# Optimization experiments

Measured on AMD Instinct MI355X. Metric: run time of the kernel, lower is better.

The kernel has to match this reference:

```python
import jax, jax.numpy as jnp
import numpy as np
import math

HID = 128
NH = 8
HD = HID // NH
NL = 3
CLIP = 10.0
EPS = 1e-5

def _ln(x, g, b):
    mu = jnp.mean(x, axis=-1, keepdims=True)
    var = jnp.var(x, axis=-1, keepdims=True)
    return (x - mu) * jax.lax.rsqrt(var + EPS) * g + b

def _layer(h, e_bias1, e_gate2, g1, b1, wh, g2, b2, w1, w2):
    B, N, _ = h.shape
    h_in = h
    hn = _ln(h, g1, b1)
    qkv = hn @ wh                                   # (B,N,3H)
    q, k, v = jnp.split(qkv, 3, axis=-1)
    q = q.reshape(B, N, NH, HD).transpose(0, 2, 1, 3)  # (B,nh,N,hd)
    k = k.reshape(B, N, NH, HD).transpose(0, 2, 1, 3)
    v = v.reshape(B, N, NH, HD).transpose(0, 2, 1, 3)
    att = jnp.einsum('bhid,bhjd->bhij', q, k) * (1.0 / math.sqrt(HD))
    att = jax.nn.softmax(att + e_bias1, axis=-1) * e_gate2
    y = jnp.einsum('bhij,bhjd->bhid', att, v)
    y = y.transpose(0, 2, 1, 3).reshape(B, N, HID)
    z = _ln(y + h_in, g2, b2)
    mlp = jax.nn.relu(z @ w1) @ w2
    return mlp + y

def setup_inputs() -> dict:
    key = jax.random.key(0)
    ks = jax.random.split(key, 9)
    d = {
        'node_features': jax.random.normal(ks[0], (16, 256, 2), jnp.float32),
        'edge_features': jax.random.normal(ks[1], (16, 256, 256, 1), jnp.float32),
        'Wn': jax.random.normal(ks[2], (2, HID), jnp.float32) * 0.5,
        'We_in': jax.random.normal(ks[3], (1, HID), jnp.float32) * 0.1,
        'ln1_g': jnp.ones((NL, HID), jnp.float32),
        'ln1_b': jnp.zeros((NL, HID), jnp.float32),
        'Wh': jax.random.normal(ks[4], (NL, HID, 3 * HID), jnp.float32) * (1.0 / math.sqrt(HID)),
        'We': jax.random.normal(ks[5], (NL, HID, 2 * NH), jnp.float32) * (1.0 / math.sqrt(HID)),
        'ln2_g': jnp.ones((NL, HID), jnp.float32),
        'ln2_b': jnp.zeros((NL, HID), jnp.float32),
        'W1': jax.random.normal(ks[6], (NL, HID, 4 * HID), jnp.float32) * (1.0 / math.sqrt(HID)),
        'W2': jax.random.normal(ks[7], (NL, 4 * HID, HID), jnp.float32) * (1.0 / math.sqrt(4 * HID)),
        'Wdec': jax.random.normal(ks[8], (HID, 1), jnp.float32) * (1.0 / math.sqrt(HID)),
    }
    return d

def reference(node_features, edge_features, Wn, We_in, ln1_g, ln1_b, Wh, We, ln2_g, ln2_b, W1, W2, Wdec):
    h = node_features @ Wn                              # (B,N,H)
    e = edge_features @ We_in                           # (B,N,N,H)
    for i in range(NL):
        ee = e @ We[i]                                  # (B,N,N,2*nh)
        ee = ee.transpose(0, 3, 1, 2)                   # (B,2*nh,N,N)
        e1, e2 = ee[:, :NH], ee[:, NH:]
        h = _layer(h, e1, e2, ln1_g[i], ln1_b[i], Wh[i], ln2_g[i], ln2_b[i], W1[i], W2[i])
    out = h @ Wdec                                      # (B,N,1)
    out = CLIP * jnp.tanh(out / math.sqrt(HID))
    return out
```

## Files before the change

### kernel.cpp

```cpp
#include <hip/hip_runtime.h>
#include <math.h>

#define HID 128
#define NHEAD 8
#define NL 3
#define NS 256
#define ROWS 4096

typedef __attribute__((ext_vector_type(8))) short bf16x8;
typedef __attribute__((ext_vector_type(4))) float f32x4;

__device__ __forceinline__ float us2f(unsigned short s) { return __uint_as_float(((unsigned)s) << 16); }
__device__ __forceinline__ unsigned short f2b(float f) {
    unsigned u = __float_as_uint(f);
    return (unsigned short)((u + 0x7fff + ((u >> 16) & 1)) >> 16);
}

__global__ __launch_bounds__(256) void k_prep(
    const float* __restrict__ Wh, const float* __restrict__ W1, const float* __restrict__ W2,
    const float* __restrict__ We_in, const float* __restrict__ We,
    const float* __restrict__ nf, const float* __restrict__ Wn,
    unsigned short* __restrict__ WhH, unsigned short* __restrict__ WhL,
    unsigned short* __restrict__ W1H, unsigned short* __restrict__ W1L,
    unsigned short* __restrict__ W2H, unsigned short* __restrict__ W2L,
    float* __restrict__ sbuf, float* __restrict__ h)
{
    int b = blockIdx.x, t = threadIdx.x;
    if (b >= 529) {
        int idx = (b - 529) * 256 + t;
        int r = idx >> 7, c = idx & 127;
        h[idx] = nf[2 * r] * Wn[c] + nf[2 * r + 1] * Wn[HID + c];
        return;
    }
    if (b == 528) {
        if (t < NL * 2 * NHEAD) {
            int l = t / (2 * NHEAD), j = t % (2 * NHEAD);
            float acc = 0.f;
            for (int c = 0; c < HID; ++c)
                acc += We_in[c] * We[(long)(l * HID + c) * (2 * NHEAD) + j];
            sbuf[t] = acc;
        }
        return;
    }
    const float* S; unsigned short *OH, *OL; int K, N, kt, nt;
    if (b < 144) {
        int l = b / 48, rem = b % 48; kt = rem & 3; nt = rem >> 2; K = 128; N = 384;
        S = Wh + (long)l * 128 * 384; OH = WhH + (long)l * 384 * 128; OL = WhL + (long)l * 384 * 128;
    } else if (b < 336) {
        int b2 = b - 144; int l = b2 / 64, rem = b2 % 64; kt = rem & 3; nt = rem >> 2; K = 128; N = 512;
        S = W1 + (long)l * 128 * 512; OH = W1H + (long)l * 512 * 128; OL = W1L + (long)l * 512 * 128;
    } else {
        int b2 = b - 336; int l = b2 / 64, rem = b2 % 64; kt = rem & 15; nt = rem >> 4; K = 512; N = 128;
        S = W2 + (long)l * 512 * 128; OH = W2H + (long)l * 128 * 512; OL = W2L + (long)l * 128 * 512;
    }
    __shared__ float sm[32][33];
    int i0 = t >> 5, j = t & 31;
#pragma unroll
    for (int p = 0; p < 4; ++p) {
        int i = i0 + p * 8;
        sm[i][j] = S[(long)(kt * 32 + i) * N + nt * 32 + j];
    }
    __syncthreads();
#pragma unroll
    for (int p = 0; p < 4; ++p) {
        int n = i0 + p * 8;
        float v = sm[j][n];
        unsigned short hh = f2b(v);
        long o = (long)(nt * 32 + n) * K + kt * 32 + j;
        OH[o] = hh; OL[o] = f2b(v - us2f(hh));
    }
}

__global__ __launch_bounds__(256) void k_fgemm(
    const float* __restrict__ x, const float* __restrict__ x2,
    const float* __restrict__ g, const float* __restrict__ b,
    const unsigned short* __restrict__ WH, const unsigned short* __restrict__ WL,
    unsigned short* __restrict__ Ch, unsigned short* __restrict__ Cl,
    int Nc, int mode)
{
    __shared__ unsigned short sAh[64 * 136], sAl[64 * 136];
    __shared__ unsigned short sWh[64 * 136], sWl[64 * 136];
    int t = threadIdx.x;
    int row0 = blockIdx.y * 64, col0 = blockIdx.x * 64;

#pragma unroll
    for (int p = 0; p < 4; ++p) {
        int rr = (t >> 4) + p * 16, ck = t & 15;
        *(uint4*)&sWh[rr * 136 + ck * 8] = *(const uint4*)&WH[(long)(col0 + rr) * 128 + ck * 8];
        *(uint4*)&sWl[rr * 136 + ck * 8] = *(const uint4*)&WL[(long)(col0 + rr) * 128 + ck * 8];
    }
#pragma unroll
    for (int pass = 0; pass < 2; ++pass) {
        int row = pass * 32 + (t >> 3);
        int p = t & 7, cb = p * 16;
        float v[16];
        const float* xp = x + (long)(row0 + row) * HID + cb;
#pragma unroll
        for (int j = 0; j < 16; j += 4) *(float4*)&v[j] = *(const float4*)(xp + j);
        if (x2) {
            const float* yp = x2 + (long)(row0 + row) * HID + cb;
#pragma unroll
            for (int j = 0; j < 16; j += 4) {
                float4 r4 = *(const float4*)(yp + j);
                v[j] += r4.x; v[j+1] += r4.y; v[j+2] += r4.z; v[j+3] += r4.w;
            }
        }
        float s = 0.f, s2 = 0.f;
#pragma unroll
        for (int j = 0; j < 16; ++j) { s += v[j]; s2 += v[j] * v[j]; }
        s  += __shfl_xor(s, 1);  s  += __shfl_xor(s, 2);  s  += __shfl_xor(s, 4);
        s2 += __shfl_xor(s2, 1); s2 += __shfl_xor(s2, 2); s2 += __shfl_xor(s2, 4);
        float mu  = s * (1.f / HID);
        float var = s2 * (1.f / HID) - mu * mu;
        float inv = rsqrtf(var + 1e-5f);
        unsigned short hi[16], lo[16];
#pragma unroll
        for (int j = 0; j < 16; ++j) {
            int c = cb + j;
            float o = (v[j] - mu) * inv * g[c] + b[c];
            hi[j] = f2b(o); lo[j] = f2b(o - us2f(hi[j]));
        }
        *(uint4*)&sAh[row * 136 + cb]     = *(uint4*)&hi[0];
        *(uint4*)&sAh[row * 136 + cb + 8] = *(uint4*)&hi[8];
        *(uint4*)&sAl[row * 136 + cb]     = *(uint4*)&lo[0];
        *(uint4*)&sAl[row * 136 + cb + 8] = *(uint4*)&lo[8];
    }
    __syncthreads();

    int w = t >> 6, lane = t & 63;
    int m = lane & 15, quad = lane >> 4;
    f32x4 acc[4];
#pragma unroll
    for (int i = 0; i < 4; ++i) acc[i] = (f32x4){0.f, 0.f, 0.f, 0.f};
#pragma unroll
    for (int c = 0; c < 4; ++c) {
        bf16x8 ah = *(const bf16x8*)&sAh[(w * 16 + m) * 136 + c * 32 + quad * 8];
        bf16x8 al = *(const bf16x8*)&sAl[(w * 16 + m) * 136 + c * 32 + quad * 8];
#pragma unroll
        for (int nt = 0; nt < 4; ++nt) {
            bf16x8 wh = *(const bf16x8*)&sWh[(nt * 16 + m) * 136 + c * 32 + quad * 8];
            bf16x8 wl = *(const bf16x8*)&sWl[(nt * 16 + m) * 136 + c * 32 + quad * 8];
            acc[nt] = __builtin_amdgcn_mfma_f32_16x16x32_bf16(ah, wh, acc[nt], 0, 0, 0);
            acc[nt] = __builtin_amdgcn_mfma_f32_16x16x32_bf16(ah, wl, acc[nt], 0, 0, 0);
            acc[nt] = __builtin_amdgcn_mfma_f32_16x16x32_bf16(al, wh, acc[nt], 0, 0, 0);
        }
    }
#pragma unroll
    for (int nt = 0; nt < 4; ++nt) {
#pragma unroll
        for (int r = 0; r < 4; ++r) {
            int row = row0 + w * 16 + quad * 4 + r;
            int col = col0 + nt * 16 + m;
            float v = acc[nt][r];
            if (mode) v = fmaxf(v, 0.f);
            unsigned short hh = f2b(v);
            Ch[(long)row * Nc + col] = hh;
            Cl[(long)row * Nc + col] = f2b(v - us2f(hh));
        }
    }
}

__global__ __launch_bounds__(512, 1) void k_mlp(
    const float* __restrict__ y, const float* __restrict__ h,
    const float* __restrict__ g, const float* __restrict__ b,
    const unsigned short* __restrict__ W1H_, const unsigned short* __restrict__ W1L_,
    const unsigned short* __restrict__ W2H_, const unsigned short* __restrict__ W2L_,
    float* __restrict__ hout, const float* __restrict__ Wdec, float* __restrict__ out)
{
    __shared__ __align__(16) unsigned short sAh[16 * 136], sAl[16 * 136];
    __shared__ __align__(16) unsigned short sHh[16 * 520], sHl[16 * 520];
    int t = threadIdx.x;
    int row0 = blockIdx.x * 16;
    int w = t >> 6, lane = t & 63;
    int m = lane & 15, quad = lane >> 4;

    const unsigned short* w1h = W1H_ + (long)(w * 64 + m) * 128 + quad * 8;
    const unsigned short* w1l = W1L_ + (long)(w * 64 + m) * 128 + quad * 8;
    bf16x8 p1h[4], p1l[4];
#pragma unroll
    for (int nt = 0; nt < 4; ++nt) {
        p1h[nt] = *(const bf16x8*)&w1h[nt * 16 * 128];
        p1l[nt] = *(const bf16x8*)&w1l[nt * 16 * 128];
    }

    {
        int row = t >> 5, cb = (t & 31) * 4;
        float4 a4 = *(const float4*)&y[(long)(row0 + row) * HID + cb];
        float4 b4 = *(const float4*)&h[(long)(row0 + row) * HID + cb];
        float v[4] = {a4.x + b4.x, a4.y + b4.y, a4.z + b4.z, a4.w + b4.w};
        float s = v[0] + v[1] + v[2] + v[3];
        float s2 = v[0]*v[0] + v[1]*v[1] + v[2]*v[2] + v[3]*v[3];
        s  += __shfl_xor(s, 1);  s  += __shfl_xor(s, 2);  s  += __shfl_xor(s, 4);
        s  += __shfl_xor(s, 8);  s  += __shfl_xor(s, 16);
        s2 += __shfl_xor(s2, 1); s2 += __shfl_xor(s2, 2); s2 += __shfl_xor(s2, 4);
        s2 += __shfl_xor(s2, 8); s2 += __shfl_xor(s2, 16);
        float mu  = s * (1.f / HID);
        float var = s2 * (1.f / HID) - mu * mu;
        float inv = rsqrtf(var + 1e-5f);
        unsigned short hi4[4], lo4[4];
#pragma unroll
        for (int j = 0; j < 4; ++j) {
            int c = cb + j;
            float o = (v[j] - mu) * inv * g[c] + b[c];
            hi4[j] = f2b(o); lo4[j] = f2b(o - us2f(hi4[j]));
        }
        *(uint2*)&sAh[row * 136 + cb] = *(const uint2*)hi4;
        *(uint2*)&sAl[row * 136 + cb] = *(const uint2*)lo4;
    }
    __syncthreads();

    f32x4 acc1[4];
#pragma unroll
    for (int i = 0; i < 4; ++i) acc1[i] = (f32x4){0.f, 0.f, 0.f, 0.f};
#pragma unroll
    for (int c = 0; c < 4; ++c) {
        bf16x8 ah = *(const bf16x8*)&sAh[m * 136 + c * 32 + quad * 8];
        bf16x8 al = *(const bf16x8*)&sAl[m * 136 + c * 32 + quad * 8];
#pragma unroll
        for (int nt = 0; nt < 4; ++nt) {
            bf16x8 wh = (c == 0) ? p1h[nt] : *(const bf16x8*)&w1h[nt * 16 * 128 + c * 32];
            bf16x8 wl = (c == 0) ? p1l[nt] : *(const bf16x8*)&w1l[nt * 16 * 128 + c * 32];
            acc1[nt] = __builtin_amdgcn_mfma_f32_16x16x32_bf16(wh, ah, acc1[nt], 0, 0, 0);
            acc1[nt] = __builtin_amdgcn_mfma_f32_16x16x32_bf16(wh, al, acc1[nt], 0, 0, 0);
            acc1[nt] = __builtin_amdgcn_mfma_f32_16x16x32_bf16(wl, ah, acc1[nt], 0, 0, 0);
        }
    }
#pragma unroll
    for (int nt = 0; nt < 4; ++nt) {
        unsigned short hi4[4], lo4[4];
#pragma unroll
        for (int r = 0; r < 4; ++r) {
            float v = fmaxf(acc1[nt][r], 0.f);
            hi4[r] = f2b(v);
            lo4[r] = f2b(v - us2f(hi4[r]));
        }
        int kk = w * 64 + nt * 16 + quad * 4;
        *(uint2*)&sHh[m * 520 + kk] = *(const uint2*)hi4;
        *(uint2*)&sHl[m * 520 + kk] = *(const uint2*)lo4;
    }

    const unsigned short* w2h = W2H_ + (long)(w * 16 + m) * 512 + quad * 8;
    const unsigned short* w2l = W2L_ + (long)(w * 16 + m) * 512 + quad * 8;
    bf16x8 p2h = *(const bf16x8*)w2h;
    bf16x8 p2l = *(const bf16x8*)w2l;
    __syncthreads();

    f32x4 acc2 = (f32x4){0.f, 0.f, 0.f, 0.f};
#pragma unroll
    for (int c = 0; c < 16; ++c) {
        bf16x8 ah = *(const bf16x8*)&sHh[m * 520 + c * 32 + quad * 8];
        bf16x8 al = *(const bf16x8*)&sHl[m * 520 + c * 32 + quad * 8];
        bf16x8 wh = (c == 0) ? p2h : *(const bf16x8*)&w2h[c * 32];
        bf16x8 wl = (c == 0) ? p2l : *(const bf16x8*)&w2l[c * 32];
        acc2 = __builtin_amdgcn_mfma_f32_16x16x32_bf16(ah, wh, acc2, 0, 0, 0);
        acc2 = __builtin_amdgcn_mfma_f32_16x16x32_bf16(ah, wl, acc2, 0, 0, 0);
        acc2 = __builtin_amdgcn_mfma_f32_16x16x32_bf16(al, wh, acc2, 0, 0, 0);
    }
    __syncthreads();
    float* ht = (float*)&sHh[0];
#pragma unroll
    for (int r = 0; r < 4; ++r) {
        int row = quad * 4 + r;
        int col = w * 16 + m;
        float v = acc2[r] + y[(long)(row0 + row) * HID + col];
        hout[(long)(row0 + row) * HID + col] = v;
        ht[row * 132 + col] = v;
    }
    __syncthreads();
    if (Wdec && t < 256) {
        int row = t >> 4, sub = t & 15;
        float vv[8];
        *(float4*)&vv[0] = *(const float4*)&ht[row * 132 + sub * 8];
        *(float4*)&vv[4] = *(const float4*)&ht[row * 132 + sub * 8 + 4];
        float a = 0.f;
#pragma unroll
        for (int j = 0; j < 8; ++j) a += vv[j] * Wdec[sub * 8 + j];
        a += __shfl_xor(a, 1); a += __shfl_xor(a, 2); a += __shfl_xor(a, 4); a += __shfl_xor(a, 8);
        if (sub == 0) out[row0 + row] = 10.f * tanhf(a * 0.08838834764831845f);
    }
}

#define PAS 268
#define KQS 20
__global__ __launch_bounds__(256) void k_attn(
    const unsigned short* __restrict__ qkvH, const unsigned short* __restrict__ qkvL,
    const float* __restrict__ ef, const float* __restrict__ sbuf,
    int layer, float* __restrict__ y)
{
    __shared__ unsigned short Kh[NS * KQS], Kl[NS * KQS];
    __shared__ unsigned short Qh[64 * KQS], Ql[64 * KQS];
    __shared__ unsigned short Vh[16 * PAS], Vl[16 * PAS];
    __shared__ unsigned short Pa[4][16 * PAS];
    int bid = blockIdx.x;
    int q4 = bid & 3, hh = (bid >> 2) & 7, bb = bid >> 5;
    int t = threadIdx.x;
    {
        long kb = ((long)(bb * NS + t)) * 384 + HID + hh * 16;
        union { uint4 u[2]; unsigned short s[16]; } KH, KL, VH, VL;
        KH.u[0] = *(const uint4*)&qkvH[kb];       KH.u[1] = *(const uint4*)&qkvH[kb + 8];
        KL.u[0] = *(const uint4*)&qkvL[kb];       KL.u[1] = *(const uint4*)&qkvL[kb + 8];
        VH.u[0] = *(const uint4*)&qkvH[kb + 128]; VH.u[1] = *(const uint4*)&qkvH[kb + 136];
        VL.u[0] = *(const uint4*)&qkvL[kb + 128]; VL.u[1] = *(const uint4*)&qkvL[kb + 136];
#pragma unroll
        for (int d = 0; d < 16; ++d) {
            Kh[t * KQS + d] = KH.s[d];
            Kl[t * KQS + d] = KL.s[d];
            Vh[d * PAS + t] = VH.s[d];
            Vl[d * PAS + t] = VL.s[d];
        }
    }
    {
        int row = t >> 2, c4 = (t & 3) * 4;
        long qb = ((long)(bb * NS + q4 * 64 + row)) * 384 + hh * 16 + c4;
        union { uint2 u; unsigned short s[4]; } QH, QL;
        QH.u = *(const uint2*)&qkvH[qb];
        QL.u = *(const uint2*)&qkvL[qb];
#pragma unroll
        for (int j = 0; j < 4; ++j) {
            Qh[row * KQS + c4 + j] = QH.s[j];
            Ql[row * KQS + c4 + j] = QL.s[j];
        }
    }
    __syncthreads();
    int w = t >> 6, lane = t & 63;
    int m = lane & 15, quad = lane >> 4;
    float s1  = sbuf[layer * 16 + hh];
    float s2g = sbuf[layer * 16 + NHEAD + hh];
    unsigned short* Paw = Pa[w];

    bf16x8 qh = (bf16x8){0,0,0,0,0,0,0,0}, ql = qh;
    if (quad < 2) {
        qh = *(const bf16x8*)&Qh[(w * 16 + m) * KQS + quad * 8];
        ql = *(const bf16x8*)&Ql[(w * 16 + m) * KQS + quad * 8];
    }
    f32x4 sc[16];
#pragma unroll
    for (int ct = 0; ct < 16; ++ct) {
        bf16x8 kh = (bf16x8){0,0,0,0,0,0,0,0}, kl = kh;
        if (quad < 2) {
            kh = *(const bf16x8*)&Kh[(ct * 16 + m) * KQS + quad * 8];
            kl = *(const bf16x8*)&Kl[(ct * 16 + m) * KQS + quad * 8];
        }
        f32x4 a = (f32x4){0.f, 0.f, 0.f, 0.f};
        a = __builtin_amdgcn_mfma_f32_16x16x32_bf16(qh, kh, a, 0, 0, 0);
        a = __builtin_amdgcn_mfma_f32_16x16x32_bf16(qh, kl, a, 0, 0, 0);
        a = __builtin_amdgcn_mfma_f32_16x16x32_bf16(ql, kh, a, 0, 0, 0);
        sc[ct] = a;
    }
    int baserow = q4 * 64 + w * 16 + quad * 4;
    float s[4] = {0.f, 0.f, 0.f, 0.f};
#pragma unroll
    for (int ct = 0; ct < 16; ++ct) {
#pragma unroll
        for (int r = 0; r < 4; ++r) {
            float e = ef[((long)(bb * NS + baserow + r)) * NS + ct * 16 + m];
            float p = __expf(sc[ct][r] * 0.25f + e * s1);
            s[r] += p;
            Paw[(quad * 4 + r) * PAS + ct * 16 + m] = f2b(p * e);
        }
    }
    float inv[4];
#pragma unroll
    for (int r = 0; r < 4; ++r) {
        float ss = s[r];
        ss += __shfl_xor(ss, 1); ss += __shfl_xor(ss, 2);
        ss += __shfl_xor(ss, 4); ss += __shfl_xor(ss, 8);
        inv[r] = s2g / ss;
    }
    __syncthreads();
    f32x4 acc = (f32x4){0.f, 0.f, 0.f, 0.f};
#pragma unroll
    for (int sft = 0; sft < 8; ++sft) {
        bf16x8 pf = *(const bf16x8*)&Paw[m * PAS + sft * 32 + quad * 8];
        bf16x8 vh = *(const bf16x8*)&Vh[m * PAS + sft * 32 + quad * 8];
        bf16x8 vl = *(const bf16x8*)&Vl[m * PAS + sft * 32 + quad * 8];
        acc = __builtin_amdgcn_mfma_f32_16x16x32_bf16(pf, vh, acc, 0, 0, 0);
        acc = __builtin_amdgcn_mfma_f32_16x16x32_bf16(pf, vl, acc, 0, 0, 0);
    }
#pragma unroll
    for (int r = 0; r < 4; ++r) {
        int row = q4 * 64 + w * 16 + quad * 4 + r;
        y[((long)(bb * NS + row)) * HID + hh * 16 + m] = acc[r] * inv[r];
    }
}

extern "C" void kernel_launch(void* const* d_in, const int* in_sizes, int n_in,
                              void* d_out, int out_size, void* d_ws, size_t ws_size,
                              hipStream_t stream) {
    const float* nf    = (const float*)d_in[0];
    const float* ef    = (const float*)d_in[1];
    const float* Wn    = (const float*)d_in[2];
    const float* We_in = (const float*)d_in[3];
    const float* ln1g  = (const float*)d_in[4];
    const float* ln1b  = (const float*)d_in[5];
    const float* Wh    = (const float*)d_in[6];
    const float* We    = (const float*)d_in[7];
    const float* ln2g  = (const float*)d_in[8];
    const float* ln2b  = (const float*)d_in[9];
    const float* W1    = (const float*)d_in[10];
    const float* W2    = (const float*)d_in[11];
    const float* Wdec  = (const float*)d_in[12];

    float* ws   = (float*)d_ws;
    float* sbuf = ws;
    float* h    = ws + 64;
    float* y    = h + ROWS * HID;
    unsigned short* qkvH = (unsigned short*)(y + ROWS * HID);
    unsigned short* qkvL = qkvH + (long)ROWS * 384;
    unsigned short* WhH  = qkvL + (long)ROWS * 384;
    unsigned short* WhL  = WhH + (long)NL * 384 * 128;
    unsigned short* W1H  = WhL + (long)NL * 384 * 128;
    unsigned short* W1L  = W1H + (long)NL * 512 * 128;
    unsigned short* W2H  = W1L + (long)NL * 512 * 128;
    unsigned short* W2L  = W2H + (long)NL * 128 * 512;

    k_prep<<<529 + ROWS * HID / 256, 256, 0, stream>>>(Wh, W1, W2, We_in, We, nf, Wn,
                                    WhH, WhL, W1H, W1L, W2H, W2L, sbuf, h);
    for (int l = 0; l < NL; ++l) {
        k_fgemm<<<dim3(6, 64), 256, 0, stream>>>(h, nullptr,
            ln1g + l * HID, ln1b + l * HID,
            WhH + (long)l * 384 * 128, WhL + (long)l * 384 * 128,
            qkvH, qkvL, 384, 0);
        k_attn<<<512, 256, 0, stream>>>(qkvH, qkvL, ef, sbuf, l, y);
        int last = (l == NL - 1);
        k_mlp<<<ROWS / 16, 512, 0, stream>>>(y, h,
            ln2g + l * HID, ln2b + l * HID,
            W1H + (long)l * 512 * 128, W1L + (long)l * 512 * 128,
            W2H + (long)l * 128 * 512, W2L + (long)l * 128 * 512,
            h, last ? Wdec : nullptr, (float*)d_out);
    }
}
```

Measured before the change: 208.0 us.

## Restructure QKV GEMM as row-tile kernel, prefetch weights and edge features

Replaces the 64x64-tiled QKV GEMM with a 16-row-per-block kernel. Its 8 waves each stream their own 48-column weight slice straight from global memory into registers, so the LayerNorm is computed once per row and no weights are staged in LDS. The MLP GEMMs and the attention score loop now double-buffer their next weight fragments and edge-feature values in registers, to hide global-load latency behind the MFMA work. A __syncthreads before the P·V stage in attention is removed. That relies on each wave reading only its own Paw rows and on V already being synchronized, and costs more registers.

```diff
diff --git a/kernel.cpp b/kernel.cpp
--- a/kernel.cpp
+++ b/kernel.cpp
@@ -71,92 +71,87 @@
     }
 }
 
-__global__ __launch_bounds__(256) void k_fgemm(
-    const float* __restrict__ x, const float* __restrict__ x2,
+__global__ __launch_bounds__(512, 1) void k_qkv(
+    const float* __restrict__ x,
     const float* __restrict__ g, const float* __restrict__ b,
     const unsigned short* __restrict__ WH, const unsigned short* __restrict__ WL,
-    unsigned short* __restrict__ Ch, unsigned short* __restrict__ Cl,
-    int Nc, int mode)
+    unsigned short* __restrict__ Ch, unsigned short* __restrict__ Cl)
 {
-    __shared__ unsigned short sAh[64 * 136], sAl[64 * 136];
-    __shared__ unsigned short sWh[64 * 136], sWl[64 * 136];
+    __shared__ __align__(16) unsigned short sAh[16 * 136], sAl[16 * 136];
     int t = threadIdx.x;
-    int row0 = blockIdx.y * 64, col0 = blockIdx.x * 64;
-
-#pragma unroll
-    for (int p = 0; p < 4; ++p) {
-        int rr = (t >> 4) + p * 16, ck = t & 15;
-        *(uint4*)&sWh[rr * 136 + ck * 8] = *(const uint4*)&WH[(long)(col0 + rr) * 128 + ck * 8];
-        *(uint4*)&sWl[rr * 136 + ck * 8] = *(const uint4*)&WL[(long)(col0 + rr) * 128 + ck * 8];
-    }
-#pragma unroll
-    for (int pass = 0; pass < 2; ++pass) {
-        int row = pass * 32 + (t >> 3);
-        int p = t & 7, cb = p * 16;
-        float v[16];
-        const float* xp = x + (long)(row0 + row) * HID + cb;
-#pragma unroll
-        for (int j = 0; j < 16; j += 4) *(float4*)&v[j] = *(const float4*)(xp + j);
-        if (x2) {
-            const float* yp = x2 + (long)(row0 + row) * HID + cb;
-#pragma unroll
-            for (int j = 0; j < 16; j += 4) {
-                float4 r4 = *(const float4*)(yp + j);
-                v[j] += r4.x; v[j+1] += r4.y; v[j+2] += r4.z; v[j+3] += r4.w;
-            }
-        }
-        float s = 0.f, s2 = 0.f;
-#pragma unroll
-        for (int j = 0; j < 16; ++j) { s += v[j]; s2 += v[j] * v[j]; }
+    int row0 = blockIdx.x * 16;
+    int w = t >> 6, lane = t & 63;
+    int m = lane & 15, quad = lane >> 4;
+
+    const unsigned short* wh0 = WH + (long)(w * 48 + m) * 128 + quad * 8;
+    const unsigned short* wl0 = WL + (long)(w * 48 + m) * 128 + quad * 8;
+    bf16x8 f1h[3], f1l[3];
+#pragma unroll
+    for (int nt = 0; nt < 3; ++nt) {
+        f1h[nt] = *(const bf16x8*)&wh0[nt * 16 * 128];
+        f1l[nt] = *(const bf16x8*)&wl0[nt * 16 * 128];
+    }
+
+    {
+        int row = t >> 5, cb = (t & 31) * 4;
+        float4 a4 = *(const float4*)&x[(long)(row0 + row) * HID + cb];
+        float v[4] = {a4.x, a4.y, a4.z, a4.w};
+        float s = v[0] + v[1] + v[2] + v[3];
+        float s2 = v[0]*v[0] + v[1]*v[1] + v[2]*v[2] + v[3]*v[3];
         s  += __shfl_xor(s, 1);  s  += __shfl_xor(s, 2);  s  += __shfl_xor(s, 4);
+        s  += __shfl_xor(s, 8);  s  += __shfl_xor(s, 16);
         s2 += __shfl_xor(s2, 1); s2 += __shfl_xor(s2, 2); s2 += __shfl_xor(s2, 4);
+        s2 += __shfl_xor(s2, 8); s2 += __shfl_xor(s2, 16);
         float mu  = s * (1.f / HID);
         float var = s2 * (1.f / HID) - mu * mu;
         float inv = rsqrtf(var + 1e-5f);
-        unsigned short hi[16], lo[16];
-#pragma unroll
-        for (int j = 0; j < 16; ++j) {
+        unsigned short hi4[4], lo4[4];
+#pragma unroll
+        for (int j = 0; j < 4; ++j) {
             int c = cb + j;
             float o = (v[j] - mu) * inv * g[c] + b[c];
-            hi[j] = f2b(o); lo[j] = f2b(o - us2f(hi[j]));
-        }
-        *(uint4*)&sAh[row * 136 + cb]     = *(uint4*)&hi[0];
-        *(uint4*)&sAh[row * 136 + cb + 8] = *(uint4*)&hi[8];
-        *(uint4*)&sAl[row * 136 + cb]     = *(uint4*)&lo[0];
-        *(uint4*)&sAl[row * 136 + cb + 8] = *(uint4*)&lo[8];
-    }
-    __syncthreads();
-
-    int w = t >> 6, lane = t & 63;
-    int m = lane & 15, quad = lane >> 4;
-    f32x4 acc[4];
-#pragma unroll
-    for (int i = 0; i < 4; ++i) acc[i] = (f32x4){0.f, 0.f, 0.f, 0.f};
+            hi4[j] = f2b(o); lo4[j] = f2b(o - us2f(hi4[j]));
+        }
+        *(uint2*)&sAh[row * 136 + cb] = *(const uint2*)hi4;
+        *(uint2*)&sAl[row * 136 + cb] = *(const uint2*)lo4;
+    }
+    __syncthreads();
+
+    f32x4 acc[3];
+#pragma unroll
+    for (int i = 0; i < 3; ++i) acc[i] = (f32x4){0.f, 0.f, 0.f, 0.f};
 #pragma unroll
     for (int c = 0; c < 4; ++c) {
-        bf16x8 ah = *(const bf16x8*)&sAh[(w * 16 + m) * 136 + c * 32 + quad * 8];
-        bf16x8 al = *(const bf16x8*)&sAl[(w * 16 + m) * 136 + c * 32 + quad * 8];
-#pragma unroll
-        for (int nt = 0; nt < 4; ++nt) {
-            bf16x8 wh = *(const bf16x8*)&sWh[(nt * 16 + m) * 136 + c * 32 + quad * 8];
-            bf16x8 wl = *(const bf16x8*)&sWl[(nt * 16 + m) * 136 + c * 32 + quad * 8];
-            acc[nt] = __builtin_amdgcn_mfma_f32_16x16x32_bf16(ah, wh, acc[nt], 0, 0, 0);
-            acc[nt] = __builtin_amdgcn_mfma_f32_16x16x32_bf16(ah, wl, acc[nt], 0, 0, 0);
-            acc[nt] = __builtin_amdgcn_mfma_f32_16x16x32_bf16(al, wh, acc[nt], 0, 0, 0);
-        }
-    }
-#pragma unroll
-    for (int nt = 0; nt < 4; ++nt) {
+        bf16x8 n1h[3] = {}, n1l[3] = {};
+        if (c < 3) {
+#pragma unroll
+            for (int nt = 0; nt < 3; ++nt) {
+                n1h[nt] = *(const bf16x8*)&wh0[nt * 16 * 128 + (c + 1) * 32];
+                n1l[nt] = *(const bf16x8*)&wl0[nt * 16 * 128 + (c + 1) * 32];
+            }
+        }
+        bf16x8 ah = *(const bf16x8*)&sAh[m * 136 + c * 32 + quad * 8];
+        bf16x8 al = *(const bf16x8*)&sAl[m * 136 + c * 32 + quad * 8];
+#pragma unroll
+        for (int nt = 0; nt < 3; ++nt) {
+            acc[nt] = __builtin_amdgcn_mfma_f32_16x16x32_bf16(f1h[nt], ah, acc[nt], 0, 0, 0);
+            acc[nt] = __builtin_amdgcn_mfma_f32_16x16x32_bf16(f1h[nt], al, acc[nt], 0, 0, 0);
+            acc[nt] = __builtin_amdgcn_mfma_f32_16x16x32_bf16(f1l[nt], ah, acc[nt], 0, 0, 0);
+        }
+#pragma unroll
+        for (int nt = 0; nt < 3; ++nt) { f1h[nt] = n1h[nt]; f1l[nt] = n1l[nt]; }
+    }
+#pragma unroll
+    for (int nt = 0; nt < 3; ++nt) {
+        unsigned short hi4[4], lo4[4];
 #pragma unroll
         for (int r = 0; r < 4; ++r) {
-            int row = row0 + w * 16 + quad * 4 + r;
-            int col = col0 + nt * 16 + m;
             float v = acc[nt][r];
-            if (mode) v = fmaxf(v, 0.f);
-            unsigned short hh = f2b(v);
-            Ch[(long)row * Nc + col] = hh;
-            Cl[(long)row * Nc + col] = f2b(v - us2f(hh));
-        }
+            hi4[r] = f2b(v); lo4[r] = f2b(v - us2f(hi4[r]));
+        }
+        long o = (long)(row0 + m) * 384 + w * 48 + nt * 16 + quad * 4;
+        *(uint2*)&Ch[o] = *(const uint2*)hi4;
+        *(uint2*)&Cl[o] = *(const uint2*)lo4;
     }
 }
 
@@ -176,11 +171,11 @@
 
     const unsigned short* w1h = W1H_ + (long)(w * 64 + m) * 128 + quad * 8;
     const unsigned short* w1l = W1L_ + (long)(w * 64 + m) * 128 + quad * 8;
-    bf16x8 p1h[4], p1l[4];
+    bf16x8 f1h[4], f1l[4];
 #pragma unroll
     for (int nt = 0; nt < 4; ++nt) {
-        p1h[nt] = *(const bf16x8*)&w1h[nt * 16 * 128];
-        p1l[nt] = *(const bf16x8*)&w1l[nt * 16 * 128];
+        f1h[nt] = *(const bf16x8*)&w1h[nt * 16 * 128];
+        f1l[nt] = *(const bf16x8*)&w1l[nt * 16 * 128];
     }
 
     {
@@ -214,16 +209,24 @@
     for (int i = 0; i < 4; ++i) acc1[i] = (f32x4){0.f, 0.f, 0.f, 0.f};
 #pragma unroll
     for (int c = 0; c < 4; ++c) {
+        bf16x8 n1h[4] = {}, n1l[4] = {};
+        if (c < 3) {
+#pragma unroll
+            for (int nt = 0; nt < 4; ++nt) {
+                n1h[nt] = *(const bf16x8*)&w1h[nt * 16 * 128 + (c + 1) * 32];
+                n1l[nt] = *(const bf16x8*)&w1l[nt * 16 * 128 + (c + 1) * 32];
+            }
+        }
         bf16x8 ah = *(const bf16x8*)&sAh[m * 136 + c * 32 + quad * 8];
         bf16x8 al = *(const bf16x8*)&sAl[m * 136 + c * 32 + quad * 8];
 #pragma unroll
         for (int nt = 0; nt < 4; ++nt) {
-            bf16x8 wh = (c == 0) ? p1h[nt] : *(const bf16x8*)&w1h[nt * 16 * 128 + c * 32];
-            bf16x8 wl = (c == 0) ? p1l[nt] : *(const bf16x8*)&w1l[nt * 16 * 128 + c * 32];
-            acc1[nt] = __builtin_amdgcn_mfma_f32_16x16x32_bf16(wh, ah, acc1[nt], 0, 0, 0);
-            acc1[nt] = __builtin_amdgcn_mfma_f32_16x16x32_bf16(wh, al, acc1[nt], 0, 0, 0);
-            acc1[nt] = __builtin_amdgcn_mfma_f32_16x16x32_bf16(wl, ah, acc1[nt], 0, 0, 0);
-        }
+            acc1[nt] = __builtin_amdgcn_mfma_f32_16x16x32_bf16(f1h[nt], ah, acc1[nt], 0, 0, 0);
+            acc1[nt] = __builtin_amdgcn_mfma_f32_16x16x32_bf16(f1h[nt], al, acc1[nt], 0, 0, 0);
+            acc1[nt] = __builtin_amdgcn_mfma_f32_16x16x32_bf16(f1l[nt], ah, acc1[nt], 0, 0, 0);
+        }
+#pragma unroll
+        for (int nt = 0; nt < 4; ++nt) { f1h[nt] = n1h[nt]; f1l[nt] = n1l[nt]; }
     }
 #pragma unroll
     for (int nt = 0; nt < 4; ++nt) {
@@ -241,20 +244,24 @@
 
     const unsigned short* w2h = W2H_ + (long)(w * 16 + m) * 512 + quad * 8;
     const unsigned short* w2l = W2L_ + (long)(w * 16 + m) * 512 + quad * 8;
-    bf16x8 p2h = *(const bf16x8*)w2h;
-    bf16x8 p2l = *(const bf16x8*)w2l;
+    bf16x8 cwh = *(const bf16x8*)w2h;
+    bf16x8 cwl = *(const bf16x8*)w2l;
     __syncthreads();
 
     f32x4 acc2 = (f32x4){0.f, 0.f, 0.f, 0.f};
 #pragma unroll
     for (int c = 0; c < 16; ++c) {
+        bf16x8 nwh = {}, nwl = {};
+        if (c < 15) {
+            nwh = *(const bf16x8*)&w2h[(c + 1) * 32];
+            nwl = *(const bf16x8*)&w2l[(c + 1) * 32];
+        }
         bf16x8 ah = *(const bf16x8*)&sHh[m * 520 + c * 32 + quad * 8];
         bf16x8 al = *(const bf16x8*)&sHl[m * 520 + c * 32 + quad * 8];
-        bf16x8 wh = (c == 0) ? p2h : *(const bf16x8*)&w2h[c * 32];
-        bf16x8 wl = (c == 0) ? p2l : *(const bf16x8*)&w2l[c * 32];
-        acc2 = __builtin_amdgcn_mfma_f32_16x16x32_bf16(ah, wh, acc2, 0, 0, 0);
-        acc2 = __builtin_amdgcn_mfma_f32_16x16x32_bf16(ah, wl, acc2, 0, 0, 0);
-        acc2 = __builtin_amdgcn_mfma_f32_16x16x32_bf16(al, wh, acc2, 0, 0, 0);
+        acc2 = __builtin_amdgcn_mfma_f32_16x16x32_bf16(ah, cwh, acc2, 0, 0, 0);
+        acc2 = __builtin_amdgcn_mfma_f32_16x16x32_bf16(ah, cwl, acc2, 0, 0, 0);
+        acc2 = __builtin_amdgcn_mfma_f32_16x16x32_bf16(al, cwh, acc2, 0, 0, 0);
+        cwh = nwh; cwl = nwl;
     }
     __syncthreads();
     float* ht = (float*)&sHh[0];
@@ -333,7 +340,12 @@
         qh = *(const bf16x8*)&Qh[(w * 16 + m) * KQS + quad * 8];
         ql = *(const bf16x8*)&Ql[(w * 16 + m) * KQS + quad * 8];
     }
-    f32x4 sc[16];
+    int baserow = q4 * 64 + w * 16 + quad * 4;
+    const float* efp = ef + ((long)(bb * NS + baserow)) * NS + m;
+    float s[4] = {0.f, 0.f, 0.f, 0.f};
+    float e0[4], e1[4];
+#pragma unroll
+    for (int r = 0; r < 4; ++r) e0[r] = efp[r * NS];
 #pragma unroll
     for (int ct = 0; ct < 16; ++ct) {
         bf16x8 kh = (bf16x8){0,0,0,0,0,0,0,0}, kl = kh;
@@ -345,19 +357,19 @@
         a = __builtin_amdgcn_mfma_f32_16x16x32_bf16(qh, kh, a, 0, 0, 0);
         a = __builtin_amdgcn_mfma_f32_16x16x32_bf16(qh, kl, a, 0, 0, 0);
         a = __builtin_amdgcn_mfma_f32_16x16x32_bf16(ql, kh, a, 0, 0, 0);
-        sc[ct] = a;
-    }
-    int baserow = q4 * 64 + w * 16 + quad * 4;
-    float s[4] = {0.f, 0.f, 0.f, 0.f};
-#pragma unroll
-    for (int ct = 0; ct < 16; ++ct) {
+        e1[0] = e1[1] = e1[2] = e1[3] = 0.f;
+        if (ct < 15) {
+#pragma unroll
+            for (int r = 0; r < 4; ++r) e1[r] = efp[r * NS + (ct + 1) * 16];
+        }
 #pragma unroll
         for (int r = 0; r < 4; ++r) {
-            float e = ef[((long)(bb * NS + baserow + r)) * NS + ct * 16 + m];
-            float p = __expf(sc[ct][r] * 0.25f + e * s1);
+            float p = __expf(a[r] * 0.25f + e0[r] * s1);
             s[r] += p;
-            Paw[(quad * 4 + r) * PAS + ct * 16 + m] = f2b(p * e);
-        }
+            Paw[(quad * 4 + r) * PAS + ct * 16 + m] = f2b(p * e0[r]);
+        }
+#pragma unroll
+        for (int r = 0; r < 4; ++r) e0[r] = e1[r];
     }
     float inv[4];
 #pragma unroll
@@ -367,7 +379,6 @@
         ss += __shfl_xor(ss, 4); ss += __shfl_xor(ss, 8);
         inv[r] = s2g / ss;
     }
-    __syncthreads();
     f32x4 acc = (f32x4){0.f, 0.f, 0.f, 0.f};
 #pragma unroll
     for (int sft = 0; sft < 8; ++sft) {
@@ -417,10 +428,10 @@
     k_prep<<<529 + ROWS * HID / 256, 256, 0, stream>>>(Wh, W1, W2, We_in, We, nf, Wn,
                                     WhH, WhL, W1H, W1L, W2H, W2L, sbuf, h);
     for (int l = 0; l < NL; ++l) {
-        k_fgemm<<<dim3(6, 64), 256, 0, stream>>>(h, nullptr,
+        k_qkv<<<ROWS / 16, 512, 0, stream>>>(h,
             ln1g + l * HID, ln1b + l * HID,
             WhH + (long)l * 384 * 128, WhL + (long)l * 384 * 128,
-            qkvH, qkvL, 384, 0);
+            qkvH, qkvL);
         k_attn<<<512, 256, 0, stream>>>(qkvH, qkvL, ef, sbuf, l, y);
         int last = (l == NL - 1);
         k_mlp<<<ROWS / 16, 512, 0, stream>>>(y, h,
```

Result: slower. 215.0 us (+3.3%).

## Store qkv feature-major to vectorize GEMM stores and V staging in attention

Applied to the files above, without the earlier changes.

The QKV projection output is stored transposed (feature-major, token-contiguous). The GEMM epilogue can then write four consecutive rows as one 8-byte store, and attention can stage V into shared memory with vector stores. Q and K are now scattered into their row-major LDS tiles with scalar stores. A redundant barrier before the PV product is dropped because each wave reads only its own P buffer and V was already synchronized.

```diff
diff --git a/kernel.cpp b/kernel.cpp
--- a/kernel.cpp
+++ b/kernel.cpp
@@ -76,7 +76,7 @@
     const float* __restrict__ g, const float* __restrict__ b,
     const unsigned short* __restrict__ WH, const unsigned short* __restrict__ WL,
     unsigned short* __restrict__ Ch, unsigned short* __restrict__ Cl,
-    int Nc, int mode)
+    int mode)
 {
     __shared__ unsigned short sAh[64 * 136], sAl[64 * 136];
     __shared__ unsigned short sWh[64 * 136], sWl[64 * 136];
@@ -147,16 +147,16 @@
     }
 #pragma unroll
     for (int nt = 0; nt < 4; ++nt) {
+        unsigned short hi4[4], lo4[4];
 #pragma unroll
         for (int r = 0; r < 4; ++r) {
-            int row = row0 + w * 16 + quad * 4 + r;
-            int col = col0 + nt * 16 + m;
             float v = acc[nt][r];
             if (mode) v = fmaxf(v, 0.f);
-            unsigned short hh = f2b(v);
-            Ch[(long)row * Nc + col] = hh;
-            Cl[(long)row * Nc + col] = f2b(v - us2f(hh));
-        }
+            hi4[r] = f2b(v); lo4[r] = f2b(v - us2f(hi4[r]));
+        }
+        long o = (long)(col0 + nt * 16 + m) * ROWS + row0 + w * 16 + quad * 4;
+        *(uint2*)&Ch[o] = *(const uint2*)hi4;
+        *(uint2*)&Cl[o] = *(const uint2*)lo4;
     }
 }
 
@@ -295,30 +295,35 @@
     int q4 = bid & 3, hh = (bid >> 2) & 7, bb = bid >> 5;
     int t = threadIdx.x;
     {
-        long kb = ((long)(bb * NS + t)) * 384 + HID + hh * 16;
+        int d = t >> 4, kc = (t & 15) * 16;
+        long base = (long)ROWS * (HID + hh * 16 + d) + bb * NS + kc;
+        long vbase = base + (long)ROWS * 128;
         union { uint4 u[2]; unsigned short s[16]; } KH, KL, VH, VL;
-        KH.u[0] = *(const uint4*)&qkvH[kb];       KH.u[1] = *(const uint4*)&qkvH[kb + 8];
-        KL.u[0] = *(const uint4*)&qkvL[kb];       KL.u[1] = *(const uint4*)&qkvL[kb + 8];
-        VH.u[0] = *(const uint4*)&qkvH[kb + 128]; VH.u[1] = *(const uint4*)&qkvH[kb + 136];
-        VL.u[0] = *(const uint4*)&qkvL[kb + 128]; VL.u[1] = *(const uint4*)&qkvL[kb + 136];
-#pragma unroll
-        for (int d = 0; d < 16; ++d) {
-            Kh[t * KQS + d] = KH.s[d];
-            Kl[t * KQS + d] = KL.s[d];
-            Vh[d * PAS + t] = VH.s[d];
-            Vl[d * PAS + t] = VL.s[d];
+        KH.u[0] = *(const uint4*)&qkvH[base];      KH.u[1] = *(const uint4*)&qkvH[base + 8];
+        KL.u[0] = *(const uint4*)&qkvL[base];      KL.u[1] = *(const uint4*)&qkvL[base + 8];
+        VH.u[0] = *(const uint4*)&qkvH[vbase];     VH.u[1] = *(const uint4*)&qkvH[vbase + 8];
+        VL.u[0] = *(const uint4*)&qkvL[vbase];     VL.u[1] = *(const uint4*)&qkvL[vbase + 8];
+#pragma unroll
+        for (int j = 0; j < 16; ++j) {
+            Kh[(kc + j) * KQS + d] = KH.s[j];
+            Kl[(kc + j) * KQS + d] = KL.s[j];
+        }
+#pragma unroll
+        for (int j = 0; j < 4; ++j) {
+            *(uint2*)&Vh[d * PAS + kc + j * 4] = *(const uint2*)&VH.s[j * 4];
+            *(uint2*)&Vl[d * PAS + kc + j * 4] = *(const uint2*)&VL.s[j * 4];
         }
     }
     {
-        int row = t >> 2, c4 = (t & 3) * 4;
-        long qb = ((long)(bb * NS + q4 * 64 + row)) * 384 + hh * 16 + c4;
+        int d = t >> 4, rc = (t & 15) * 4;
+        long qb = (long)ROWS * (hh * 16 + d) + bb * NS + q4 * 64 + rc;
         union { uint2 u; unsigned short s[4]; } QH, QL;
         QH.u = *(const uint2*)&qkvH[qb];
         QL.u = *(const uint2*)&qkvL[qb];
 #pragma unroll
         for (int j = 0; j < 4; ++j) {
-            Qh[row * KQS + c4 + j] = QH.s[j];
-            Ql[row * KQS + c4 + j] = QL.s[j];
+            Qh[(rc + j) * KQS + d] = QH.s[j];
+            Ql[(rc + j) * KQS + d] = QL.s[j];
         }
     }
     __syncthreads();
@@ -367,7 +372,6 @@
         ss += __shfl_xor(ss, 4); ss += __shfl_xor(ss, 8);
         inv[r] = s2g / ss;
     }
-    __syncthreads();
     f32x4 acc = (f32x4){0.f, 0.f, 0.f, 0.f};
 #pragma unroll
     for (int sft = 0; sft < 8; ++sft) {
@@ -406,8 +410,8 @@
     float* h    = ws + 64;
     float* y    = h + ROWS * HID;
     unsigned short* qkvH = (unsigned short*)(y + ROWS * HID);
-    unsigned short* qkvL = qkvH + (long)ROWS * 384;
-    unsigned short* WhH  = qkvL + (long)ROWS * 384;
+    unsigned short* qkvL = qkvH + (long)384 * ROWS;
+    unsigned short* WhH  = qkvL + (long)384 * ROWS;
     unsigned short* WhL  = WhH + (long)NL * 384 * 128;
     unsigned short* W1H  = WhL + (long)NL * 384 * 128;
     unsigned short* W1L  = W1H + (long)NL * 512 * 128;
@@ -420,7 +424,7 @@
         k_fgemm<<<dim3(6, 64), 256, 0, stream>>>(h, nullptr,
             ln1g + l * HID, ln1b + l * HID,
             WhH + (long)l * 384 * 128, WhL + (long)l * 384 * 128,
-            qkvH, qkvL, 384, 0);
+            qkvH, qkvL, 0);
         k_attn<<<512, 256, 0, stream>>>(qkvH, qkvL, ef, sbuf, l, y);
         int last = (l == NL - 1);
         k_mlp<<<ROWS / 16, 512, 0, stream>>>(y, h,
```

After: 202.8 us. 2.5% less time.
